# Optimization experiments

Hardware: AMD Instinct MI355X
Metric: run time of the kernel (lower is better)

The kernel has to match this reference:

```python
import jax, jax.numpy as jnp
import numpy as np
from math import factorial

LMAX = 5
MUL = 128            # multiplicity per irrep degree in the node embedding
NUM_CHANNELS = 4
NUM_RADII = 64
RES_BETA = 180
RES_ALPHA = 359
NUM_SPECIES = 5
NUM_GRAPHS = 16
NUM_NODES = 512
SH_DIM = (LMAX + 1) ** 2          # 36
EMB_DIM = MUL * SH_DIM            # 4608
NUM_IRREPS = MUL * (LMAX + 1)     # 768
INV_TEMP = 1.0


def _real_sh_basis(lmax, res_beta, res_alpha):
    """Orthonormal real spherical harmonics evaluated on a Gauss-Legendre beta grid
    and a uniform alpha grid (the grid used by e3nn.to_s2grid with gausslegendre
    quadrature). Returns B[(l*l + l + m), beta, alpha]. Precomputed in numpy since
    the grid is static."""
    y, _ = np.polynomial.legendre.leggauss(res_beta)          # y = cos(beta)
    alpha = np.linspace(0.0, 2.0 * np.pi, res_alpha, endpoint=False)
    # associated Legendre P[l, m] on y (Condon-Shortley phase)
    P = np.zeros((lmax + 1, lmax + 1, res_beta))
    P[0, 0] = 1.0
    somx2 = np.sqrt(np.clip(1.0 - y * y, 0.0, None))
    for m in range(1, lmax + 1):
        P[m, m] = -(2 * m - 1) * somx2 * P[m - 1, m - 1]
    for m in range(lmax):
        P[m + 1, m] = (2 * m + 1) * y * P[m, m]
    for m in range(lmax + 1):
        for l in range(m + 2, lmax + 1):
            P[l, m] = ((2 * l - 1) * y * P[l - 1, m] - (l + m - 1) * P[l - 2, m]) / (l - m)
    B = np.zeros(((lmax + 1) ** 2, res_beta, res_alpha))
    ones_a = np.ones_like(alpha)
    for l in range(lmax + 1):
        for m in range(l + 1):
            N = np.sqrt((2 * l + 1) / (4.0 * np.pi) * factorial(l - m) / factorial(l + m))
            if m == 0:
                B[l * l + l] = (N * P[l, 0])[:, None] * ones_a[None, :]
            else:
                B[l * l + l + m] = np.sqrt(2.0) * N * P[l, m][:, None] * np.cos(m * alpha)[None, :]
                B[l * l + l - m] = np.sqrt(2.0) * N * P[l, m][:, None] * np.sin(m * alpha)[None, :]
    return jnp.asarray(B, dtype=jnp.float32)


_B = _real_sh_basis(LMAX, RES_BETA, RES_ALPHA)   # (36, 180, 359)


def _split_blocks(emb):
    """Split an irreps array (G, sum_l MUL*(2l+1)) into per-degree blocks (G, MUL, 2l+1)."""
    blocks, off = [], 0
    for l in range(LMAX + 1):
        d = 2 * l + 1
        blocks.append(emb[:, off:off + MUL * d].reshape(-1, MUL, d))
        off += MUL * d
    return blocks


def setup_inputs() -> dict:
    key = jax.random.key(0)
    ks = jax.random.split(key, 13)
    inp = {
        "node_embeddings": jax.random.normal(ks[0], (NUM_NODES, EMB_DIM), jnp.float32),
        "species_embed": jax.random.normal(ks[1], (NUM_SPECIES, NUM_IRREPS), jnp.float32),
        "W_radial": jax.random.normal(ks[2], (MUL, NUM_RADII), jnp.float32),
        "W_mlp1": jax.random.normal(ks[3], (NUM_RADII, MUL), jnp.float32),
        "W_mlp2": jax.random.normal(ks[4], (MUL, NUM_RADII), jnp.float32),
    }
    for l in range(LMAX + 1):
        inp[f"W_ang_{l}"] = jax.random.normal(ks[5 + l], (MUL, NUM_CHANNELS), jnp.float32)
    inp["focus_indices"] = jax.random.randint(ks[11], (NUM_GRAPHS,), 0, NUM_NODES)
    inp["target_species"] = jax.random.randint(ks[12], (NUM_GRAPHS,), 0, NUM_SPECIES)
    return inp


def _forward(node_embeddings, species_embed, W_radial, W_mlp1, W_mlp2, W_ang,
             focus_indices, target_species):
    rsqrt_mul = np.float32(1.0 / np.sqrt(MUL))
    focus = node_embeddings[focus_indices]                 # (G, EMB_DIM)
    spec = species_embed[target_species]                   # (G, NUM_IRREPS), one scalar per irrep
    blocks = _split_blocks(focus)
    # target_species_embeddings * focus_node_embeddings: scale each irrep by its scalar
    scaled = [blk * spec[:, MUL * l:MUL * (l + 1), None] for l, blk in enumerate(blocks)]
    # radial path: e3nn Linear to num_radii x 0e (only 0e inputs contribute) + MLP
    scal0 = scaled[0][..., 0]                              # (G, MUL)
    r = (scal0 @ W_radial) * rsqrt_mul                     # (G, NUM_RADII)
    h = jax.nn.softplus((r @ W_mlp1) * np.float32(1.0 / np.sqrt(NUM_RADII)))
    radial_logits = (h @ W_mlp2) * rsqrt_mul               # (G, NUM_RADII)
    # angular path: e3nn Linear to num_channels * s2_irreps (per-degree channel mixing)
    ang = jnp.concatenate(
        [jnp.einsum("gkm,kc->gcm", scaled[l], W_ang[l]) * rsqrt_mul
         for l in range(LMAX + 1)], axis=-1)               # (G, C, 36)
    # joint distribution coefficients: radial logit adds to the l=0 coefficient
    joint0 = ang[:, :, None, :1] + radial_logits[:, None, :, None]     # (G, C, R, 1)
    rest = jnp.broadcast_to(ang[:, :, None, 1:],
                            (NUM_GRAPHS, NUM_CHANNELS, NUM_RADII, SH_DIM - 1))
    log_position_coeffs = jnp.concatenate([joint0, rest], axis=-1) * np.float32(INV_TEMP)
    # log_coeffs_to_logits: SH synthesis on the grid, then logsumexp over channels
    pos_grid = jnp.einsum("gcrk,kba->gcrba", log_position_coeffs, _B)
    position_logits = jax.nn.logsumexp(pos_grid, axis=1)   # (G, R, beta, alpha)
    ang_grid = jnp.einsum("gck,kba->gcba", ang, _B)
    angular_logits = jax.nn.logsumexp(ang_grid, axis=1, keepdims=True)  # (G, 1, beta, alpha)
    return log_position_coeffs, position_logits, angular_logits, radial_logits


def reference(node_embeddings, species_embed, W_radial, W_mlp1, W_mlp2,
              W_ang_0, W_ang_1, W_ang_2, W_ang_3, W_ang_4, W_ang_5,
              focus_indices, target_species):
    W_ang = [W_ang_0, W_ang_1, W_ang_2, W_ang_3, W_ang_4, W_ang_5]
    return _forward(node_embeddings, species_embed, W_radial, W_mlp1, W_mlp2, W_ang,
                    focus_indices, target_species)
```

## Files before the change

### kernel.cpp

```cpp
#include <hip/hip_runtime.h>
#include <math.h>

#define LMAX   5
#define MUL    128
#define NCH    4
#define NRAD   64
#define RBETA  180
#define RALPHA 359
#define NGRAPH 16
#define SH_DIM 36
#define EMB_DIM 4608
#define NIRR   768

#define GRID_BA (RBETA * RALPHA)
#define N_F4    (GRID_BA / 4)
#define NW21    21

typedef float vfloat4 __attribute__((ext_vector_type(4)));

#define OUT0_OFF 0
#define OUT1_OFF 147456
#define OUT2_OFF (147456 + 66170880)
#define OUT3_OFF (147456 + 66170880 + 1033920)

#define WS_TAB_OFF 0
#define WS_ANG_OFF 15360
#define WS_RAD_OFF 24576

__global__ __launch_bounds__(256)
void k_small(const float* __restrict__ ne, const float* __restrict__ sp,
             const float* __restrict__ wrad, const float* __restrict__ wm1,
             const float* __restrict__ wm2,
             const float* __restrict__ wa0, const float* __restrict__ wa1,
             const float* __restrict__ wa2, const float* __restrict__ wa3,
             const float* __restrict__ wa4, const float* __restrict__ wa5,
             const int* __restrict__ focus, const int* __restrict__ tspec,
             float* __restrict__ out0, float* __restrict__ out3,
             float* __restrict__ ang_ws, float* __restrict__ rad_ws,
             float* __restrict__ tab)
{
    const int tid = threadIdx.x;

    if (blockIdx.x == NGRAPH) {
        __shared__ double rcp[RBETA];
        for (int k = tid; k < RBETA; k += 256) rcp[k] = 1.0 / (double)(k + 1);
        __syncthreads();
        const int i = tid;
        if (i >= RBETA) return;
        const double PI = 3.14159265358979323846;
        double x = -cos(PI * (i + 0.75) / (RBETA + 0.5));
        for (int it = 0; it < 4; ++it) {
            double p0 = 1.0, p1 = x;
            for (int k = 1; k < RBETA; ++k) {
                double p2 = ((2.0 * k + 1.0) * x * p1 - (double)k * p0) * rcp[k];
                p0 = p1; p1 = p2;
            }
            double dp = RBETA * (x * p1 - p0) / (x * x - 1.0);
            x -= p1 / dp;
        }
        double P[LMAX + 1][LMAX + 1];
        P[0][0] = 1.0;
        double somx2 = sqrt(fmax(1.0 - x * x, 0.0));
        for (int m = 1; m <= LMAX; ++m) P[m][m] = -(2.0 * m - 1.0) * somx2 * P[m - 1][m - 1];
        for (int m = 0; m < LMAX; ++m)  P[m + 1][m] = (2.0 * m + 1.0) * x * P[m][m];
        for (int m = 0; m <= LMAX; ++m)
            for (int l = m + 2; l <= LMAX; ++l)
                P[l][m] = ((2.0 * l - 1.0) * x * P[l - 1][m] - (l + m - 1.0) * P[l - 2][m]) / (double)(l - m);
        const double FOURPI = 12.566370614359172;
        for (int l = 0; l <= LMAX; ++l) {
            for (int m = 0; m <= l; ++m) {
                double fr = 1.0;
                for (int k = l - m + 1; k <= l + m; ++k) fr /= (double)k;
                double N = sqrt((2.0 * l + 1.0) / FOURPI * fr);
                double w = N * P[l][m];
                if (m > 0) w *= 1.4142135623730951;
                tab[i * NW21 + l * (l + 1) / 2 + m] = (float)w;
            }
        }
        return;
    }

    __shared__ float s0[MUL];
    __shared__ float rr[NRAD];
    __shared__ float hh[MUL];
    __shared__ float rl[NRAD];
    __shared__ float sang[NCH * SH_DIM];

    const int g = blockIdx.x;
    const int fi = focus[g];
    const int ts = tspec[g];
    const float rs128 = 0.08838834764831845f;
    const float rs64  = 0.125f;

    if (tid < MUL) s0[tid] = ne[(size_t)fi * EMB_DIM + tid] * sp[ts * NIRR + tid];
    __syncthreads();

    if (tid < NRAD) {
        float acc = 0.f;
        for (int k = 0; k < MUL; ++k) acc += s0[k] * wrad[k * NRAD + tid];
        rr[tid] = acc * rs128;
    }
    __syncthreads();

    if (tid < MUL) {
        float acc = 0.f;
        for (int j = 0; j < NRAD; ++j) acc += rr[j] * wm1[j * MUL + tid];
        float x = acc * rs64;
        hh[tid] = fmaxf(x, 0.f) + log1pf(expf(-fabsf(x)));
    }
    __syncthreads();

    if (tid < NRAD) {
        float acc = 0.f;
        for (int k = 0; k < MUL; ++k) acc += hh[k] * wm2[k * NRAD + tid];
        float v = acc * rs128;
        rl[tid] = v;
        out3[g * NRAD + tid] = v;
        rad_ws[g * NRAD + tid] = v;
    }

    const float* WA[6] = {wa0, wa1, wa2, wa3, wa4, wa5};
    for (int t = tid; t < NCH * SH_DIM; t += blockDim.x) {
        int c = t / SH_DIM, kk = t % SH_DIM;
        int l = 0;
        while ((l + 1) * (l + 1) <= kk) ++l;
        int j = kk - l * l;
        int d = 2 * l + 1;
        const float* w  = WA[l];
        const float* nb = ne + (size_t)fi * EMB_DIM + MUL * l * l + j;
        const float* sb = sp + ts * NIRR + MUL * l;
        float acc = 0.f;
        for (int k = 0; k < MUL; ++k) acc += nb[k * d] * sb[k] * w[k * NCH + c];
        float v = acc * rs128;
        sang[t] = v;
        ang_ws[g * (NCH * SH_DIM) + t] = v;
    }
    __syncthreads();

    for (int t = tid; t < NCH * NRAD * SH_DIM; t += blockDim.x) {
        int kk = t % SH_DIM;
        int r  = (t / SH_DIM) % NRAD;
        int c  = t / (SH_DIM * NRAD);
        float v = sang[c * SH_DIM + kk];
        if (kk == 0) v += rl[r];
        out0[(size_t)g * (NCH * NRAD * SH_DIM) + t] = v;
    }
}

__global__ __launch_bounds__(256)
void k_angular(const float* __restrict__ tab, const float* __restrict__ ang_ws,
               float* __restrict__ out2)
{
    __shared__ float sW[NW21];
    __shared__ float sAng[NCH * SH_DIM];
    __shared__ float sF[NCH][11];

    const int beta = blockIdx.x;
    const int g    = blockIdx.y;
    const int tid  = threadIdx.x;

    if (tid < NW21) sW[tid] = tab[beta * NW21 + tid];
    for (int t = tid; t < NCH * SH_DIM; t += 256)
        sAng[t] = ang_ws[g * (NCH * SH_DIM) + t];
    __syncthreads();

    if (tid < NCH * 11) {
        int c = tid / 11, j = tid % 11;
        float acc = 0.f;
        if (j == 0) {
            for (int l = 0; l <= LMAX; ++l)
                acc += sAng[c * SH_DIM + l * l + l] * sW[l * (l + 1) / 2];
        } else if (j <= 5) {
            int m = j;
            for (int l = m; l <= LMAX; ++l)
                acc += sAng[c * SH_DIM + l * l + l + m] * sW[l * (l + 1) / 2 + m];
        } else {
            int m = j - 5;
            for (int l = m; l <= LMAX; ++l)
                acc += sAng[c * SH_DIM + l * l + l - m] * sW[l * (l + 1) / 2 + m];
        }
        sF[c][j] = acc;
    }
    __syncthreads();

    const float dalpha = 6.283185307179586f / 359.0f;
    for (int a = tid; a < RALPHA; a += 256) {
        float alpha = dalpha * (float)a;
        float s1, c1;
        __sincosf(alpha, &s1, &c1);
        float t0 = sF[0][0], t1 = sF[1][0], t2 = sF[2][0], t3 = sF[3][0];
        float cm = c1, sm = s1;
        for (int m = 1; m <= 5; ++m) {
            t0 += sF[0][m] * cm + sF[0][5 + m] * sm;
            t1 += sF[1][m] * cm + sF[1][5 + m] * sm;
            t2 += sF[2][m] * cm + sF[2][5 + m] * sm;
            t3 += sF[3][m] * cm + sF[3][5 + m] * sm;
            float cn = cm * c1 - sm * s1;
            float sn = sm * c1 + cm * s1;
            cm = cn; sm = sn;
        }
        float mx = fmaxf(fmaxf(t0, t1), fmaxf(t2, t3));
        float s = expf(t0 - mx) + expf(t1 - mx) + expf(t2 - mx) + expf(t3 - mx);
        out2[(size_t)g * GRID_BA + beta * RALPHA + a] = mx + logf(s);
    }
}

__global__ __launch_bounds__(256)
void k_pos(const float* __restrict__ out2, const float* __restrict__ rad_ws,
           float* __restrict__ out1)
{
    __shared__ float sRC[NRAD];
    const int g   = blockIdx.y;
    const int tid = threadIdx.x;
    if (tid < NRAD) sRC[tid] = rad_ws[g * NRAD + tid] * 0.28209479177387814f;
    __syncthreads();

    const int i = blockIdx.x * 256 + tid;
    if (i >= N_F4) return;
    const vfloat4 v = __builtin_nontemporal_load(
        (const vfloat4*)(out2 + (size_t)g * GRID_BA) + i);
    vfloat4* base = (vfloat4*)(out1 + (size_t)g * NRAD * GRID_BA) + i;
    #pragma unroll 16
    for (int r = 0; r < NRAD; ++r) {
        const vfloat4 w = v + sRC[r];
        __builtin_nontemporal_store(w, base + (size_t)r * N_F4);
    }
}

extern "C" void kernel_launch(void* const* d_in, const int* in_sizes, int n_in,
                              void* d_out, int out_size, void* d_ws, size_t ws_size,
                              hipStream_t stream) {
    const float* ne   = (const float*)d_in[0];
    const float* sp   = (const float*)d_in[1];
    const float* wrad = (const float*)d_in[2];
    const float* wm1  = (const float*)d_in[3];
    const float* wm2  = (const float*)d_in[4];
    const float* wa0  = (const float*)d_in[5];
    const float* wa1  = (const float*)d_in[6];
    const float* wa2  = (const float*)d_in[7];
    const float* wa3  = (const float*)d_in[8];
    const float* wa4  = (const float*)d_in[9];
    const float* wa5  = (const float*)d_in[10];
    const int* focus  = (const int*)d_in[11];
    const int* tspec  = (const int*)d_in[12];

    float* out  = (float*)d_out;
    float* out0 = out + OUT0_OFF;
    float* out1 = out + OUT1_OFF;
    float* out2 = out + OUT2_OFF;
    float* out3 = out + OUT3_OFF;

    float* tab    = (float*)((char*)d_ws + WS_TAB_OFF);
    float* ang_ws = (float*)((char*)d_ws + WS_ANG_OFF);
    float* rad_ws = (float*)((char*)d_ws + WS_RAD_OFF);

    hipLaunchKernelGGL(k_small, dim3(NGRAPH + 1), dim3(256), 0, stream,
                       ne, sp, wrad, wm1, wm2, wa0, wa1, wa2, wa3, wa4, wa5,
                       focus, tspec, out0, out3, ang_ws, rad_ws, tab);
    hipLaunchKernelGGL(k_angular, dim3(RBETA, NGRAPH), dim3(256), 0, stream,
                       tab, ang_ws, out2);
    hipLaunchKernelGGL(k_pos, dim3((N_F4 + 255) / 256, NGRAPH), dim3(256), 0, stream,
                       out2, rad_ws, out1);
}
```

Measured before the change: 347.9 us.

## Fuse angular logsumexp and radial broadcast into one beta-tiled kernel

Merges the angular grid kernel and the position-logit broadcast kernel into a single kernel that handles four beta rows per block. Each block keeps its logsumexp results in shared memory and writes both out2 and all 64 radial copies of out1 directly from there. This removes the second launch and the global re-read of out2. In exchange it gives up the nontemporal stores, gets fewer blocks (45x16), and moves the per-block store loop to a strided pattern over 359 vec4s, so the write of roughly 265MB may use bandwidth less well.

```diff
diff --git a/kernel.cpp b/kernel.cpp
--- a/kernel.cpp
+++ b/kernel.cpp
@@ -13,8 +13,9 @@
 #define NIRR   768
 
 #define GRID_BA (RBETA * RALPHA)
-#define N_F4    (GRID_BA / 4)
 #define NW21    21
+#define BTILE   4
+#define NBT     (RBETA / BTILE)
 
 typedef float vfloat4 __attribute__((ext_vector_type(4)));
 
@@ -148,82 +149,88 @@
 }
 
 __global__ __launch_bounds__(256)
-void k_angular(const float* __restrict__ tab, const float* __restrict__ ang_ws,
-               float* __restrict__ out2)
+void k_fused(const float* __restrict__ tab, const float* __restrict__ ang_ws,
+             const float* __restrict__ rad_ws,
+             float* __restrict__ out1, float* __restrict__ out2)
 {
-    __shared__ float sW[NW21];
+    __shared__ float sW[BTILE][NW21];
     __shared__ float sAng[NCH * SH_DIM];
-    __shared__ float sF[NCH][11];
-
-    const int beta = blockIdx.x;
-    const int g    = blockIdx.y;
-    const int tid  = threadIdx.x;
-
-    if (tid < NW21) sW[tid] = tab[beta * NW21 + tid];
+    __shared__ float sF[BTILE][NCH][11];
+    __shared__ float sRC[NRAD];
+    __shared__ __align__(16) float sL[BTILE * RALPHA];
+
+    const int bt  = blockIdx.x;
+    const int g   = blockIdx.y;
+    const int tid = threadIdx.x;
+
+    if (tid < BTILE * NW21)
+        sW[tid / NW21][tid % NW21] = tab[(bt * BTILE + tid / NW21) * NW21 + tid % NW21];
+    if (tid >= 128 && tid < 128 + NRAD)
+        sRC[tid - 128] = rad_ws[g * NRAD + (tid - 128)] * 0.28209479177387814f;
     for (int t = tid; t < NCH * SH_DIM; t += 256)
         sAng[t] = ang_ws[g * (NCH * SH_DIM) + t];
     __syncthreads();
 
-    if (tid < NCH * 11) {
-        int c = tid / 11, j = tid % 11;
+    if (tid < BTILE * NCH * 11) {
+        int b = tid / (NCH * 11);
+        int rem = tid % (NCH * 11);
+        int c = rem / 11, j = rem % 11;
+        const float* W = sW[b];
         float acc = 0.f;
         if (j == 0) {
             for (int l = 0; l <= LMAX; ++l)
-                acc += sAng[c * SH_DIM + l * l + l] * sW[l * (l + 1) / 2];
+                acc += sAng[c * SH_DIM + l * l + l] * W[l * (l + 1) / 2];
         } else if (j <= 5) {
             int m = j;
             for (int l = m; l <= LMAX; ++l)
-                acc += sAng[c * SH_DIM + l * l + l + m] * sW[l * (l + 1) / 2 + m];
+                acc += sAng[c * SH_DIM + l * l + l + m] * W[l * (l + 1) / 2 + m];
         } else {
             int m = j - 5;
             for (int l = m; l <= LMAX; ++l)
-                acc += sAng[c * SH_DIM + l * l + l - m] * sW[l * (l + 1) / 2 + m];
-        }
-        sF[c][j] = acc;
+                acc += sAng[c * SH_DIM + l * l + l - m] * W[l * (l + 1) / 2 + m];
+        }
+        sF[b][c][j] = acc;
     }
     __syncthreads();
 
     const float dalpha = 6.283185307179586f / 359.0f;
-    for (int a = tid; a < RALPHA; a += 256) {
+    for (int t = tid; t < BTILE * RALPHA; t += 256) {
+        int b = t / RALPHA;
+        int a = t % RALPHA;
         float alpha = dalpha * (float)a;
         float s1, c1;
         __sincosf(alpha, &s1, &c1);
-        float t0 = sF[0][0], t1 = sF[1][0], t2 = sF[2][0], t3 = sF[3][0];
+        float t0 = sF[b][0][0], t1 = sF[b][1][0], t2 = sF[b][2][0], t3 = sF[b][3][0];
         float cm = c1, sm = s1;
         for (int m = 1; m <= 5; ++m) {
-            t0 += sF[0][m] * cm + sF[0][5 + m] * sm;
-            t1 += sF[1][m] * cm + sF[1][5 + m] * sm;
-            t2 += sF[2][m] * cm + sF[2][5 + m] * sm;
-            t3 += sF[3][m] * cm + sF[3][5 + m] * sm;
+            t0 += sF[b][0][m] * cm + sF[b][0][5 + m] * sm;
+            t1 += sF[b][1][m] * cm + sF[b][1][5 + m] * sm;
+            t2 += sF[b][2][m] * cm + sF[b][2][5 + m] * sm;
+            t3 += sF[b][3][m] * cm + sF[b][3][5 + m] * sm;
             float cn = cm * c1 - sm * s1;
             float sn = sm * c1 + cm * s1;
             cm = cn; sm = sn;
         }
         float mx = fmaxf(fmaxf(t0, t1), fmaxf(t2, t3));
         float s = expf(t0 - mx) + expf(t1 - mx) + expf(t2 - mx) + expf(t3 - mx);
-        out2[(size_t)g * GRID_BA + beta * RALPHA + a] = mx + logf(s);
-    }
-}
-
-__global__ __launch_bounds__(256)
-void k_pos(const float* __restrict__ out2, const float* __restrict__ rad_ws,
-           float* __restrict__ out1)
-{
-    __shared__ float sRC[NRAD];
-    const int g   = blockIdx.y;
-    const int tid = threadIdx.x;
-    if (tid < NRAD) sRC[tid] = rad_ws[g * NRAD + tid] * 0.28209479177387814f;
-    __syncthreads();
-
-    const int i = blockIdx.x * 256 + tid;
-    if (i >= N_F4) return;
-    const vfloat4 v = __builtin_nontemporal_load(
-        (const vfloat4*)(out2 + (size_t)g * GRID_BA) + i);
-    vfloat4* base = (vfloat4*)(out1 + (size_t)g * NRAD * GRID_BA) + i;
-    #pragma unroll 16
+        sL[t] = mx + logf(s);
+    }
+    __syncthreads();
+
+    const vfloat4* srcL = (const vfloat4*)sL;
+    const int N4 = (BTILE * RALPHA) / 4;
+
+    {
+        vfloat4* dst2 = (vfloat4*)(out2 + (size_t)g * GRID_BA + bt * (BTILE * RALPHA));
+        for (int t = tid; t < N4; t += 256)
+            dst2[t] = srcL[t];
+    }
+    float* base1 = out1 + (size_t)g * NRAD * GRID_BA + bt * (BTILE * RALPHA);
     for (int r = 0; r < NRAD; ++r) {
-        const vfloat4 w = v + sRC[r];
-        __builtin_nontemporal_store(w, base + (size_t)r * N_F4);
+        const float rc = sRC[r];
+        vfloat4* dst = (vfloat4*)(base1 + (size_t)r * GRID_BA);
+        for (int t = tid; t < N4; t += 256)
+            dst[t] = srcL[t] + rc;
     }
 }
 
@@ -257,8 +264,6 @@
     hipLaunchKernelGGL(k_small, dim3(NGRAPH + 1), dim3(256), 0, stream,
                        ne, sp, wrad, wm1, wm2, wa0, wa1, wa2, wa3, wa4, wa5,
                        focus, tspec, out0, out3, ang_ws, rad_ws, tab);
-    hipLaunchKernelGGL(k_angular, dim3(RBETA, NGRAPH), dim3(256), 0, stream,
-                       tab, ang_ws, out2);
-    hipLaunchKernelGGL(k_pos, dim3((N_F4 + 255) / 256, NGRAPH), dim3(256), 0, stream,
-                       out2, rad_ws, out1);
+    hipLaunchKernelGGL(k_fused, dim3(NBT, NGRAPH), dim3(256), 0, stream,
+                       tab, ang_ws, rad_ws, out1, out2);
 }
```

New measurement: 341.8 us, median of 2. Within noise of the previous version (-1.7%).
